# Optimization experiments

Measured on AMD Instinct MI355X. Metric: run time of the kernel, lower is better.

Reference implementation:

```python
import jax, jax.numpy as jnp
import numpy as np

EMB, HEADS = 1024, 16

def setup_inputs() -> dict:
    key = jax.random.key(0)
    ks = jax.random.split(key, 6)
    B, T, C = 2, 2048, EMB
    s = 0.02
    return {
        "x": jax.random.normal(ks[0], (B, T, C), dtype=jnp.float32),
        "Wq": jax.random.normal(ks[1], (C, C), dtype=jnp.float32) * s,
        "Wk": jax.random.normal(ks[2], (C, C), dtype=jnp.float32) * s,
        "Wv": jax.random.normal(ks[3], (C, C), dtype=jnp.float32) * s,
        "Wo": jax.random.normal(ks[4], (C, C), dtype=jnp.float32) * s,
        "bo": jnp.zeros((C,), dtype=jnp.float32),
    }

def reference(x, Wq, Wk, Wv, Wo, bo):
    B, T, C = x.shape
    H = HEADS
    S = C // H
    # torch nn.Linear: y = x @ W.T
    q = (x @ Wq.T).reshape(B, T, H, S)
    k = (x @ Wk.T).reshape(B, T, H, S)
    v = (x @ Wv.T).reshape(B, T, H, S)
    # scores [B,H,T,T]
    dot = jnp.einsum("bthd,bshd->bhts", q, k) / jnp.sqrt(jnp.float32(S))
    causal = jnp.tril(jnp.ones((T, T), dtype=bool))  # keep lower triangle
    dot = jnp.where(causal, dot, -jnp.inf)
    attn = jax.nn.softmax(dot, axis=-1)  # dropout is identity (eval / p=0)
    out = jnp.einsum("bhts,bshd->bthd", attn, v).reshape(B, T, C)
    return out @ Wo.T + bo
```

## Files before the change

kernel.cpp:

```cpp
#include <hip/hip_runtime.h>

#define BB 2
#define TT 2048
#define CC 1024
#define HH 16
#define SS 64
#define MM (BB * TT)

typedef unsigned short u16;
typedef __bf16 bf16x8 __attribute__((ext_vector_type(8)));
typedef float f32x4 __attribute__((ext_vector_type(4)));
typedef float f32x16 __attribute__((ext_vector_type(16)));

#define MFMA16(a, b, c) __builtin_amdgcn_mfma_f32_16x16x32_bf16((a), (b), (c), 0, 0, 0)
#define MFMA32(a, b, c) __builtin_amdgcn_mfma_f32_32x32x16_bf16((a), (b), (c), 0, 0, 0)
#define CVTPK(d, a, b) asm("v_cvt_pk_bf16_f32 %0, %1, %2" : "=v"(d) : "v"(a), "v"(b))

__device__ inline u16 f2bf(float f) {
    union { float f; unsigned u; } v;
    v.f = f;
    unsigned r = v.u + 0x7FFFu + ((v.u >> 16) & 1u);
    return (u16)(r >> 16);
}

__global__ __launch_bounds__(256) void cast_all(
    const float4* __restrict__ x,  const float4* __restrict__ wq,
    const float4* __restrict__ wk, const float4* __restrict__ wv,
    const float4* __restrict__ wo,
    ushort4* __restrict__ xo, ushort4* __restrict__ qo,
    ushort4* __restrict__ ko, ushort4* __restrict__ vo,
    ushort4* __restrict__ oo) {
    int bid = blockIdx.x;
    const float4* src; ushort4* dst; int i;
    if (bid < 4096) {
        src = x; dst = xo; i = bid * 256 + threadIdx.x;
    } else {
        int s = (bid - 4096) >> 10;
        int r = (bid - 4096) & 1023;
        src = (s == 0) ? wq : (s == 1) ? wk : (s == 2) ? wv : wo;
        dst = (s == 0) ? qo : (s == 1) ? ko : (s == 2) ? vo : oo;
        i = r * 256 + threadIdx.x;
    }
    float4 v = src[i];
    ushort4 o;
    o.x = f2bf(v.x); o.y = f2bf(v.y); o.z = f2bf(v.z); o.w = f2bf(v.w);
    dst[i] = o;
}

__device__ __forceinline__ void stage_tile(const u16* __restrict__ g, int row0, int k0,
                                           u16* lds) {
    int t = threadIdx.x;
#pragma unroll
    for (int q = 0; q < 2; ++q) {
        int idx = q * 256 + t;
        int row = idx >> 2;
        int chunk = (idx & 3) ^ (row & 3);
        const u16* src = g + (long)(row0 + row) * CC + k0 + chunk * 8;
        __builtin_amdgcn_global_load_lds(
            (const __attribute__((address_space(1))) void*)src,
            (__attribute__((address_space(3))) void*)(lds + idx * 8), 16, 0, 0);
    }
}

__device__ __forceinline__ void gemm_core(const u16* __restrict__ A,
                                          const u16* __restrict__ Bt,
                                          int blkM, int blkN,
                                          u16* sm,
                                          f32x4 (&acc)[4][4]) {
    int lane = threadIdx.x & 63;
    int w = threadIdx.x >> 6;
    int wr = w >> 1, wc = w & 1;
    int l15 = lane & 15;
    int hi = lane >> 4;
    const int NT = CC / 32;

    u16* bufA = sm;
    u16* bufB = sm + 3 * 4096;

#pragma unroll
    for (int m = 0; m < 4; ++m)
#pragma unroll
        for (int n = 0; n < 4; ++n) acc[m][n] = (f32x4){0.f, 0.f, 0.f, 0.f};

    stage_tile(A, blkM * 128, 0, bufA);
    stage_tile(Bt, blkN * 128, 0, bufB);
    stage_tile(A, blkM * 128, 32, bufA + 4096);
    stage_tile(Bt, blkN * 128, 32, bufB + 4096);
    stage_tile(A, blkM * 128, 64, bufA + 8192);
    stage_tile(Bt, blkN * 128, 64, bufB + 8192);

    int cur = 0;
    for (int kt = 0; kt < NT; ++kt) {
        if (kt + 2 < NT) {
            asm volatile("s_waitcnt vmcnt(8)" ::: "memory");
        } else if (kt + 1 < NT) {
            asm volatile("s_waitcnt vmcnt(4)" ::: "memory");
        } else {
            asm volatile("s_waitcnt vmcnt(0)" ::: "memory");
        }
        __builtin_amdgcn_s_barrier();
        __builtin_amdgcn_sched_barrier(0);

        u16* cA = bufA + cur * 4096;
        u16* cB = bufB + cur * 4096;

        bf16x8 af[4], bfr[4];
#pragma unroll
        for (int m = 0; m < 4; ++m) {
            int row = wr * 64 + m * 16 + l15;
            af[m] = *(const bf16x8*)(cA + row * 32 + ((hi ^ (row & 3)) << 3));
        }
#pragma unroll
        for (int n = 0; n < 4; ++n) {
            int row = wc * 64 + n * 16 + l15;
            bfr[n] = *(const bf16x8*)(cB + row * 32 + ((hi ^ (row & 3)) << 3));
        }
#pragma unroll
        for (int m = 0; m < 4; ++m)
#pragma unroll
            for (int n = 0; n < 4; ++n)
                acc[m][n] = MFMA16(af[m], bfr[n], acc[m][n]);

        __builtin_amdgcn_s_barrier();
        if (kt + 3 < NT) {
            stage_tile(A, blkM * 128, (kt + 3) * 32, cA);
            stage_tile(Bt, blkN * 128, (kt + 3) * 32, cB);
        }
        cur = (cur == 2) ? 0 : cur + 1;
    }
}

__global__ __launch_bounds__(256) void qkv_gemm(const u16* __restrict__ xb,
                                                const u16* __restrict__ wqb,
                                                const u16* __restrict__ wkb,
                                                const u16* __restrict__ wvb,
                                                u16* __restrict__ qo,
                                                u16* __restrict__ kpk,
                                                u16* __restrict__ vpk) {
    __shared__ u16 smem[6 * 128 * 32];
    int seg = blockIdx.x >> 8;
    int bid = blockIdx.x & 255;
    int blkM = bid & 31, blkN = bid >> 5;
    const u16* Bt = (seg == 0) ? wqb : (seg == 1) ? wkb : wvb;
    f32x4 acc[4][4];
    gemm_core(xb, Bt, blkM, blkN, smem, acc);

    int lane = threadIdx.x & 63;
    int w = threadIdx.x >> 6, wr = w >> 1, wc = w & 1;
    int l15 = lane & 15, hi = lane >> 4;
    int r0 = blkM * 128 + wr * 64 + hi * 4;
    int c0 = blkN * 128 + wc * 64 + l15;

    if (seg == 0) {
        const float sc = 0.18033688011112042f;
#pragma unroll
        for (int m = 0; m < 4; ++m)
#pragma unroll
            for (int n = 0; n < 4; ++n)
#pragma unroll
                for (int i = 0; i < 4; ++i)
                    qo[(long)(r0 + m * 16 + i) * CC + c0 + n * 16] =
                        f2bf(acc[m][n][i] * sc);
        return;
    }

    u16* sl = smem;
    __syncthreads();

    int ltb = wr * 64 + hi * 4;
    int lfb = wc * 64;
    if (seg == 1) {
#pragma unroll
        for (int m = 0; m < 4; ++m) {
            int lt = ltb + m * 16;
            int kvbl = lt >> 5;
#pragma unroll
            for (int n = 0; n < 4; ++n) {
                int lf = lfb + n * 16 + l15;
                int dd = lf & 63, hhl = lf >> 6;
                int base = ((kvbl << 1) + hhl) * 2048 + ((dd >> 3) << 8) + (dd & 7);
#pragma unroll
                for (int i = 0; i < 4; ++i)
                    sl[base + ((lt + i) & 31) * 8] = f2bf(acc[m][n][i]);
            }
        }
    } else {
#pragma unroll
        for (int m = 0; m < 4; ++m) {
            int lt = ltb + m * 16;
            int kvbl = lt >> 5, kv0 = lt & 31;
#pragma unroll
            for (int n = 0; n < 4; ++n) {
                int lf = lfb + n * 16 + l15;
                int dd = lf & 63, hhl = lf >> 6;
                int off = ((kvbl << 1) + hhl) * 2048 +
                          ((((dd >> 5) << 2) + (kv0 >> 3)) << 8) +
                          ((dd & 31) << 3) + (kv0 & 7);
                ushort4 p;
                p.x = f2bf(acc[m][n][0]); p.y = f2bf(acc[m][n][1]);
                p.z = f2bf(acc[m][n][2]); p.w = f2bf(acc[m][n][3]);
                *(ushort4*)(sl + off) = p;
            }
        }
    }
    __syncthreads();

    u16* pk = (seg == 1) ? kpk : vpk;
    int t = threadIdx.x;
    int b2 = blkM >> 4;
    int kvb_base = (blkM * 4) & 63;
#pragma unroll
    for (int q = 0; q < 8; ++q) {
        int kvbl = q >> 1, hhl = q & 1;
        long g = (((long)(b2 * 16 + blkN * 2 + hhl) * 64) + kvb_base + kvbl) << 11;
        bf16x8 v = *(const bf16x8*)(sl + q * 2048 + t * 8);
        *(bf16x8*)(pk + g + t * 8) = v;
    }
}

__global__ __launch_bounds__(256) void out_gemm(const u16* __restrict__ at,
                                                const u16* __restrict__ wob,
                                                const float* __restrict__ bias,
                                                float* __restrict__ out) {
    __shared__ u16 smem[6 * 128 * 32];
    int bid = blockIdx.x;
    int blkM = bid & 31, blkN = bid >> 5;
    f32x4 acc[4][4];
    gemm_core(at, wob, blkM, blkN, smem, acc);

    int lane = threadIdx.x & 63;
    int w = threadIdx.x >> 6, wr = w >> 1, wc = w & 1;
    int l15 = lane & 15, hi = lane >> 4;
    int r0 = blkM * 128 + wr * 64 + hi * 4;
    int c0 = blkN * 128 + wc * 64 + l15;
#pragma unroll
    for (int n = 0; n < 4; ++n) {
        int c = c0 + n * 16;
        float bv = bias[c];
#pragma unroll
        for (int m = 0; m < 4; ++m)
#pragma unroll
            for (int i = 0; i < 4; ++i)
                out[(long)(r0 + m * 16 + i) * CC + c] = acc[m][n][i] + bv;
    }
}

__global__ __launch_bounds__(128, 4) void attn_fwd(const u16* __restrict__ Q,
                                                   const u16* __restrict__ Kp,
                                                   const u16* __restrict__ Vp,
                                                   u16* __restrict__ O) {
    __shared__ float xch[64 * 36];
    int lane = threadIdx.x & 63;
    int w = threadIdx.x >> 6;
    int bh = blockIdx.x & 31;
    int qt = 63 - (blockIdx.x >> 5);
    int h = bh & 15, b = bh >> 4;
    int l31 = lane & 31, h5 = lane >> 5;

    int qg = qt * 32 + l31;
    int nt32 = qt + 1;

    const u16* kbase = Kp + (((long)(b * 16 + h) * 64) << 11) + h5 * 256 + l31 * 8;
    const u16* vbase = Vp + (((long)(b * 16 + h) * 64) << 11) + h5 * 256 + l31 * 8;

    const u16* qrow = Q + (long)(b * TT + qg) * CC + h * SS + h5 * 8;
    bf16x8 qf[4];
#pragma unroll
    for (int m = 0; m < 4; ++m) qf[m] = *(const bf16x8*)(qrow + m * 16);

    f32x16 oa0 = {0.f}, oa1 = {0.f};
    f32x16 ls = {0.f};

#pragma unroll 1
    for (int tt = w; tt < nt32; tt += 2) {
        const u16* kt = kbase + ((long)tt << 11);
        const u16* vt2 = vbase + ((long)tt << 11);

        bf16x8 kf0 = *(const bf16x8*)(kt);
        bf16x8 kf1 = *(const bf16x8*)(kt + 512);
        bf16x8 kf2 = *(const bf16x8*)(kt + 1024);
        bf16x8 kf3 = *(const bf16x8*)(kt + 1536);
        bf16x8 v00 = *(const bf16x8*)(vt2);
        bf16x8 v01 = *(const bf16x8*)(vt2 + 512);
        bf16x8 v10 = *(const bf16x8*)(vt2 + 1024);
        bf16x8 v11 = *(const bf16x8*)(vt2 + 1536);

        f32x16 s0 = {0.f};
        __builtin_amdgcn_s_setprio(1);
        s0 = MFMA32(kf0, qf[0], s0);
        s0 = MFMA32(kf1, qf[1], s0);
        s0 = MFMA32(kf2, qf[2], s0);
        s0 = MFMA32(kf3, qf[3], s0);
        __builtin_amdgcn_s_setprio(0);

        if (tt == qt) {
            int kvb = tt * 32 + 4 * h5;
#pragma unroll
            for (int r = 0; r < 16; ++r) {
                int kv = kvb + (r & 3) + 8 * (r >> 2);
                if (kv > qg) s0[r] = -1e30f;
            }
        }

        f32x16 p0v;
#pragma unroll
        for (int r = 0; r < 16; ++r) p0v[r] = __builtin_amdgcn_exp2f(s0[r] - 16.0f);
#pragma unroll
        for (int r = 0; r < 16; ++r) ls[r] += p0v[r];

        bf16x8 pf[2];
#pragma unroll
        for (int hk = 0; hk < 2; ++hk) {
            unsigned w0, w1, w2, w3;
            CVTPK(w0, p0v[8 * hk + 0], p0v[8 * hk + 1]);
            CVTPK(w1, p0v[8 * hk + 2], p0v[8 * hk + 3]);
            CVTPK(w2, p0v[8 * hk + 4], p0v[8 * hk + 5]);
            CVTPK(w3, p0v[8 * hk + 6], p0v[8 * hk + 7]);
            asm("v_permlane32_swap_b32 %0, %1" : "+v"(w0), "+v"(w2));
            asm("v_permlane32_swap_b32 %0, %1" : "+v"(w1), "+v"(w3));
            union { unsigned u[4]; bf16x8 v; } fb;
            fb.u[0] = w0; fb.u[1] = w1; fb.u[2] = w2; fb.u[3] = w3;
            pf[hk] = fb.v;
        }

        __builtin_amdgcn_s_setprio(1);
        oa0 = MFMA32(v00, pf[0], oa0);
        oa0 = MFMA32(v01, pf[1], oa0);
        oa1 = MFMA32(v10, pf[0], oa1);
        oa1 = MFMA32(v11, pf[1], oa1);
        __builtin_amdgcn_s_setprio(0);
    }

    float l;
    {
        float t8[8];
#pragma unroll
        for (int r = 0; r < 8; ++r) t8[r] = ls[r] + ls[r + 8];
#pragma unroll
        for (int r = 0; r < 4; ++r) t8[r] = t8[r] + t8[r + 4];
        l = (t8[0] + t8[1]) + (t8[2] + t8[3]);
        l += __shfl_xor(l, 32);
    }

    if (w == 1) {
        float* xl = xch + lane * 36;
#pragma unroll
        for (int r = 0; r < 16; ++r) { xl[r] = oa0[r]; xl[16 + r] = oa1[r]; }
        xl[32] = l;
    }
    __syncthreads();
    if (w == 0) {
        float* xl = xch + lane * 36;
        float inv = 1.0f / (l + xl[32]);

        u16* ob = O + (long)(b * TT + qg) * CC + h * SS;
#pragma unroll
        for (int rq = 0; rq < 4; ++rq) {
            float v00 = (oa0[rq * 4 + 0] + xl[rq * 4 + 0]) * inv;
            float v01 = (oa0[rq * 4 + 1] + xl[rq * 4 + 1]) * inv;
            float v02 = (oa0[rq * 4 + 2] + xl[rq * 4 + 2]) * inv;
            float v03 = (oa0[rq * 4 + 3] + xl[rq * 4 + 3]) * inv;
            float v10 = (oa1[rq * 4 + 0] + xl[16 + rq * 4 + 0]) * inv;
            float v11 = (oa1[rq * 4 + 1] + xl[16 + rq * 4 + 1]) * inv;
            float v12 = (oa1[rq * 4 + 2] + xl[16 + rq * 4 + 2]) * inv;
            float v13 = (oa1[rq * 4 + 3] + xl[16 + rq * 4 + 3]) * inv;
            unsigned a0, a1, c0, c1;
            CVTPK(a0, v00, v01);
            CVTPK(a1, v02, v03);
            CVTPK(c0, v10, v11);
            CVTPK(c1, v12, v13);
            uint2 ua, uc;
            ua.x = a0; ua.y = a1; uc.x = c0; uc.y = c1;
            *(uint2*)(ob + rq * 8 + h5 * 4) = ua;
            *(uint2*)(ob + 32 + rq * 8 + h5 * 4) = uc;
        }
    }
}

extern "C" void kernel_launch(void* const* d_in, const int* in_sizes, int n_in,
                              void* d_out, int out_size, void* d_ws, size_t ws_size,
                              hipStream_t stream) {
    const float* x  = (const float*)d_in[0];
    const float* Wq = (const float*)d_in[1];
    const float* Wk = (const float*)d_in[2];
    const float* Wv = (const float*)d_in[3];
    const float* Wo = (const float*)d_in[4];
    const float* bo = (const float*)d_in[5];

    char* ws = (char*)d_ws;
    const size_t MB = 1024 * 1024;
    u16* x_bf  = (u16*)(ws);
    u16* wq_bf = (u16*)(ws + 8 * MB);
    u16* wk_bf = (u16*)(ws + 10 * MB);
    u16* wv_bf = (u16*)(ws + 12 * MB);
    u16* wo_bf = (u16*)(ws + 14 * MB);
    u16* q_bf  = (u16*)(ws + 16 * MB);
    u16* kpack = (u16*)(ws + 24 * MB);
    u16* vpack = (u16*)(ws + 32 * MB);
    u16* at_bf = (u16*)(ws + 40 * MB);

    cast_all<<<dim3(8192), dim3(256), 0, stream>>>(
        (const float4*)x, (const float4*)Wq, (const float4*)Wk,
        (const float4*)Wv, (const float4*)Wo,
        (ushort4*)x_bf, (ushort4*)wq_bf, (ushort4*)wk_bf,
        (ushort4*)wv_bf, (ushort4*)wo_bf);

    qkv_gemm<<<dim3(768), dim3(256), 0, stream>>>(x_bf, wq_bf, wk_bf, wv_bf,
                                                  q_bf, kpack, vpack);

    attn_fwd<<<dim3(2048), dim3(128), 0, stream>>>(q_bf, kpack, vpack, at_bf);

    out_gemm<<<dim3(256), dim3(256), 0, stream>>>(at_bf, wo_bf, bo, (float*)d_out);
}
```

Measured before the change: 90.53 us.

## Widen GEMM K-tile to 64 with double buffering and 8-way XOR swizzle

Changes the shared GEMM core used by the QKV and output projections from a triple-buffered 32-wide K pipeline to a double-buffered 64-wide K pipeline. Each staged tile now holds 64 bf16 columns per row, with an 8-chunk XOR swizzle to avoid LDS bank conflicts. Each iteration runs two halves of MFMAs. This halves the number of barrier/wait iterations and issues larger loads per stage. In exchange, prefetch depth drops from two tiles ahead to one, and LDS per block grows from 48KB to 64KB, which may reduce occupancy.

```diff
diff --git a/kernel.cpp b/kernel.cpp
--- a/kernel.cpp
+++ b/kernel.cpp
@@ -47,15 +47,16 @@
     dst[i] = o;
 }
 
-__device__ __forceinline__ void stage_tile(const u16* __restrict__ g, int row0, int k0,
-                                           u16* lds) {
+__device__ __forceinline__ void stage_tile64(const u16* __restrict__ g, int row0,
+                                             int k0, u16* lds) {
     int t = threadIdx.x;
 #pragma unroll
-    for (int q = 0; q < 2; ++q) {
+    for (int q = 0; q < 4; ++q) {
         int idx = q * 256 + t;
-        int row = idx >> 2;
-        int chunk = (idx & 3) ^ (row & 3);
-        const u16* src = g + (long)(row0 + row) * CC + k0 + chunk * 8;
+        int row = idx >> 3;
+        int col = idx & 7;
+        int scol = col ^ (row & 7);
+        const u16* src = g + (long)(row0 + row) * CC + k0 + scol * 8;
         __builtin_amdgcn_global_load_lds(
             (const __attribute__((address_space(1))) void*)src,
             (__attribute__((address_space(3))) void*)(lds + idx * 8), 16, 0, 0);
@@ -72,61 +73,60 @@
     int wr = w >> 1, wc = w & 1;
     int l15 = lane & 15;
     int hi = lane >> 4;
-    const int NT = CC / 32;
+    const int NT = CC / 64;
 
     u16* bufA = sm;
-    u16* bufB = sm + 3 * 4096;
+    u16* bufB = sm + 16384;
 
 #pragma unroll
     for (int m = 0; m < 4; ++m)
 #pragma unroll
         for (int n = 0; n < 4; ++n) acc[m][n] = (f32x4){0.f, 0.f, 0.f, 0.f};
 
-    stage_tile(A, blkM * 128, 0, bufA);
-    stage_tile(Bt, blkN * 128, 0, bufB);
-    stage_tile(A, blkM * 128, 32, bufA + 4096);
-    stage_tile(Bt, blkN * 128, 32, bufB + 4096);
-    stage_tile(A, blkM * 128, 64, bufA + 8192);
-    stage_tile(Bt, blkN * 128, 64, bufB + 8192);
-
-    int cur = 0;
+    stage_tile64(A, blkM * 128, 0, bufA);
+    stage_tile64(Bt, blkN * 128, 0, bufB);
+    stage_tile64(A, blkM * 128, 64, bufA + 8192);
+    stage_tile64(Bt, blkN * 128, 64, bufB + 8192);
+
     for (int kt = 0; kt < NT; ++kt) {
-        if (kt + 2 < NT) {
+        if (kt + 1 < NT) {
             asm volatile("s_waitcnt vmcnt(8)" ::: "memory");
-        } else if (kt + 1 < NT) {
-            asm volatile("s_waitcnt vmcnt(4)" ::: "memory");
         } else {
             asm volatile("s_waitcnt vmcnt(0)" ::: "memory");
         }
         __builtin_amdgcn_s_barrier();
         __builtin_amdgcn_sched_barrier(0);
 
-        u16* cA = bufA + cur * 4096;
-        u16* cB = bufB + cur * 4096;
-
-        bf16x8 af[4], bfr[4];
-#pragma unroll
-        for (int m = 0; m < 4; ++m) {
-            int row = wr * 64 + m * 16 + l15;
-            af[m] = *(const bf16x8*)(cA + row * 32 + ((hi ^ (row & 3)) << 3));
-        }
-#pragma unroll
-        for (int n = 0; n < 4; ++n) {
-            int row = wc * 64 + n * 16 + l15;
-            bfr[n] = *(const bf16x8*)(cB + row * 32 + ((hi ^ (row & 3)) << 3));
-        }
-#pragma unroll
-        for (int m = 0; m < 4; ++m)
-#pragma unroll
-            for (int n = 0; n < 4; ++n)
-                acc[m][n] = MFMA16(af[m], bfr[n], acc[m][n]);
+        u16* cA = bufA + (kt & 1) * 8192;
+        u16* cB = bufB + (kt & 1) * 8192;
+
+#pragma unroll
+        for (int half = 0; half < 2; ++half) {
+            bf16x8 af[4], bfr[4];
+#pragma unroll
+            for (int m = 0; m < 4; ++m) {
+                int row = wr * 64 + m * 16 + l15;
+                int ch = (half * 4 + hi) ^ (row & 7);
+                af[m] = *(const bf16x8*)(cA + row * 64 + ch * 8);
+            }
+#pragma unroll
+            for (int n = 0; n < 4; ++n) {
+                int row = wc * 64 + n * 16 + l15;
+                int ch = (half * 4 + hi) ^ (row & 7);
+                bfr[n] = *(const bf16x8*)(cB + row * 64 + ch * 8);
+            }
+#pragma unroll
+            for (int m = 0; m < 4; ++m)
+#pragma unroll
+                for (int n = 0; n < 4; ++n)
+                    acc[m][n] = MFMA16(af[m], bfr[n], acc[m][n]);
+        }
 
         __builtin_amdgcn_s_barrier();
-        if (kt + 3 < NT) {
-            stage_tile(A, blkM * 128, (kt + 3) * 32, cA);
-            stage_tile(Bt, blkN * 128, (kt + 3) * 32, cB);
-        }
-        cur = (cur == 2) ? 0 : cur + 1;
+        if (kt + 2 < NT) {
+            stage_tile64(A, blkM * 128, (kt + 2) * 64, bufA + (kt & 1) * 8192);
+            stage_tile64(Bt, blkN * 128, (kt + 2) * 64, bufB + (kt & 1) * 8192);
+        }
     }
 }
 
@@ -137,7 +137,7 @@
                                                 u16* __restrict__ qo,
                                                 u16* __restrict__ kpk,
                                                 u16* __restrict__ vpk) {
-    __shared__ u16 smem[6 * 128 * 32];
+    __shared__ u16 smem[8 * 128 * 32];
     int seg = blockIdx.x >> 8;
     int bid = blockIdx.x & 255;
     int blkM = bid & 31, blkN = bid >> 5;
@@ -222,7 +222,7 @@
                                                 const u16* __restrict__ wob,
                                                 const float* __restrict__ bias,
                                                 float* __restrict__ out) {
-    __shared__ u16 smem[6 * 128 * 32];
+    __shared__ u16 smem[8 * 128 * 32];
     int bid = blockIdx.x;
     int blkM = bid & 31, blkN = bid >> 5;
     f32x4 acc[4][4];
```

Measured after the change: 82.35 us (median of 2 runs). -9.0%, faster.
